# Kernel optimization log

Hardware: AMD Instinct MI355X
Metric: run time of the kernel (lower is better)

Reference implementation:

```python
import jax, jax.numpy as jnp
import numpy as np
import math

B, V, D = 16, 4096, 512
K, H = 64, 8
DK = D // H
DE = 16
DFF = 4 * D
EPS_MASK = 1e-6
EPS_DEN = 1e-8


def setup_inputs() -> dict:
    key = jax.random.key(0)
    ks = jax.random.split(key, 16)
    s = 0.02
    return {
        "x": jax.random.normal(ks[0], (B, V, D), jnp.float32),
        "assign": jax.random.uniform(ks[1], (B, V, K), jnp.float32),
        "E": jax.random.normal(ks[2], (K, DE), jnp.float32),
        "cls0": jax.random.normal(ks[3], (1, K, D), jnp.float32) * s,
        "E2D_w": jax.random.normal(ks[4], (DE, D), jnp.float32) * s,
        "E2D_b": jnp.zeros((D,), jnp.float32),
        "Wq_w": jax.random.normal(ks[5], (D, D), jnp.float32) * s,
        "Wq_b": jnp.zeros((D,), jnp.float32),
        "Wk_w": jax.random.normal(ks[6], (D, D), jnp.float32) * s,
        "Wk_b": jnp.zeros((D,), jnp.float32),
        "Wv_w": jax.random.normal(ks[7], (D, D), jnp.float32) * s,
        "Wv_b": jnp.zeros((D,), jnp.float32),
        "ln_g": jnp.ones((D,), jnp.float32),
        "ln_b": jnp.zeros((D,), jnp.float32),
        "fc1_w": jax.random.normal(ks[8], (D, DFF), jnp.float32) * s,
        "fc1_b": jnp.zeros((DFF,), jnp.float32),
        "fc2_w": jax.random.normal(ks[9], (DFF, D), jnp.float32) * s,
        "fc2_b": jnp.zeros((D,), jnp.float32),
    }


def _layernorm(x, g, b):
    mu = x.mean(-1, keepdims=True)
    var = ((x - mu) ** 2).mean(-1, keepdims=True)
    return (x - mu) / jnp.sqrt(var + 1e-5) * g + b


def reference(x, assign, E, cls0, E2D_w, E2D_b, Wq_w, Wq_b, Wk_w, Wk_b, Wv_w, Wv_b,
              ln_g, ln_b, fc1_w, fc1_b, fc2_w, fc2_b):
    # CLS tokens modulated by module embeddings: [B,K,D]
    cls = jnp.broadcast_to(cls0, (B, K, D)) + (E @ E2D_w + E2D_b)[None]

    # detached mask (transpose of assign): [B,K,V]
    mask_kv = jax.lax.stop_gradient(jnp.swapaxes(assign, 1, 2))
    count_per_k = mask_kv.sum(-1)                 # [B,K]
    empty_mask = count_per_k <= 1e-6              # [B,K]

    # projections -> heads
    q = (_layernorm(cls, ln_g, ln_b) @ Wq_w + Wq_b).reshape(B, K, H, DK)
    k = (x @ Wk_w + Wk_b).reshape(B, V, H, DK)
    v = (x @ Wv_w + Wv_b).reshape(B, V, H, DK)

    # logits [B,H,K,V]
    logits = jnp.einsum("bkhd,bvhd->bhkv", q, k) / math.sqrt(DK)
    log_mask = jnp.log(jnp.clip(mask_kv, 0.0, 1.0) + EPS_MASK)[:, None]  # [B,1,K,V]
    scores = logits + log_mask
    scores = scores - scores.max(-1, keepdims=True)
    attn = jnp.exp(scores)
    attn = attn / (attn.sum(-1, keepdims=True) + EPS_DEN)

    # weighted values, merge heads -> [B,K,D]
    m = jnp.einsum("bhkv,bvhd->bkhd", attn, v).reshape(B, K, D)

    # empty-slot fallback
    m = jnp.where(empty_mask[..., None], cls, m)

    # FFN residual (LayerNorm shared with q path); eval mode: dropout off
    h = _layernorm(m, ln_g, ln_b)
    h = jax.nn.gelu(h @ fc1_w + fc1_b, approximate=False) @ fc2_w + fc2_b
    m = m + h
    return m, count_per_k, empty_mask
```

## Files before the change

### kernel.cpp

```cpp
#include <hip/hip_runtime.h>
#include <hip/hip_bf16.h>
#include <cstdint>
#include <cmath>

#define DEV static __device__ __forceinline__

typedef __attribute__((ext_vector_type(8))) short bf16x8;
typedef __attribute__((ext_vector_type(4))) float f32x4;

DEV ushort f2bf(float f) {
    union { float f; uint32_t u; } v; v.f = f;
    uint32_t r = v.u + 0x7FFFu + ((v.u >> 16) & 1u);
    return (ushort)(r >> 16);
}
DEV uint32_t pack2bf(float lo, float hi) {
    return (uint32_t)f2bf(lo) | ((uint32_t)f2bf(hi) << 16);
}
DEV float bf2f(ushort h) {
    union { uint32_t u; float f; } v; v.u = ((uint32_t)h) << 16;
    return v.f;
}
DEV void gld16(const ushort* g, ushort* l) {
    __builtin_amdgcn_global_load_lds(
        (const __attribute__((address_space(1))) unsigned int*)g,
        (__attribute__((address_space(3))) unsigned int*)l, 16, 0, 0);
}

__global__ __launch_bounds__(256)
void prep_all_k(int nxb, const float* __restrict__ x, ushort* __restrict__ xb,
                const float* __restrict__ E, const float* __restrict__ cls0,
                const float* __restrict__ e2dw, const float* __restrict__ e2db,
                const float* __restrict__ lng, const float* __restrict__ lnbv,
                float* __restrict__ cls, ushort* __restrict__ clsln,
                const float* __restrict__ wk, const float* __restrict__ wv,
                const float* __restrict__ fc1w, const float* __restrict__ fc2w,
                const float* __restrict__ kb, const float* __restrict__ vb,
                ushort* __restrict__ wkvt, ushort* __restrict__ fc1t,
                ushort* __restrict__ fc2t, float* __restrict__ biaskv,
                const float* __restrict__ assign, float* __restrict__ cpart)
{
    __shared__ float sh[64 * 65];
    int id = blockIdx.x;
    const int tid = threadIdx.x;

    if (id < nxb) {
        const size_t i = (size_t)id * 256 + tid;
        const float4* s = (const float4*)(x + i * 8);
        float4 a = s[0], b = s[1];
        uint4 o;
        o.x = pack2bf(a.x, a.y); o.y = pack2bf(a.z, a.w);
        o.z = pack2bf(b.x, b.y); o.w = pack2bf(b.z, b.w);
        *(uint4*)(xb + i * 8) = o;
        return;
    }
    id -= nxb;
    if (id < 64) {
        const int k = id;
        float* Ek = sh + 512;
        float2* red = (float2*)sh;
        if (tid < 16) Ek[tid] = E[k * 16 + tid];
        __syncthreads();
        float vals[2];
#pragma unroll
        for (int j = 0; j < 2; j++) {
            int d = tid + j * 256;
            float a = cls0[k * 512 + d] + e2db[d];
#pragma unroll
            for (int e = 0; e < 16; e++) a += Ek[e] * e2dw[e * 512 + d];
            vals[j] = a;
            cls[k * 512 + d] = a;
        }
        red[tid] = make_float2(vals[0] + vals[1],
                               vals[0] * vals[0] + vals[1] * vals[1]);
        __syncthreads();
        for (int s2 = 128; s2 > 0; s2 >>= 1) {
            if (tid < s2) {
                float2 o = red[tid + s2];
                float2 m = red[tid];
                red[tid] = make_float2(m.x + o.x, m.y + o.y);
            }
            __syncthreads();
        }
        float2 sr = red[0];
        float mu = sr.x * (1.f / 512.f);
        float var = sr.y * (1.f / 512.f) - mu * mu;
        float inv = rsqrtf(var + 1e-5f);
#pragma unroll
        for (int j = 0; j < 2; j++) {
            int d = tid + j * 256;
            clsln[k * 512 + d] = f2bf((vals[j] - mu) * inv * lng[d] + lnbv[d]);
        }
        return;
    }
    id -= 64;
    if (id < 2564) {
        if (id >= 2560) {
            int i = (id - 2560) * 256 + tid;
            biaskv[i] = (i < 512) ? kb[i] : vb[i - 512];
            return;
        }
        const float* in; ushort* out; int R, C, bx, by;
        if (id < 256)        { in = wk;   out = wkvt;             R = 512;  C = 512;  int t = id;        bx = t & 15; by = t >> 4; }
        else if (id < 512)   { in = wv;   out = wkvt + 512 * 512; R = 512;  C = 512;  int t = id - 256;  bx = t & 15; by = t >> 4; }
        else if (id < 1536)  { in = fc1w; out = fc1t;             R = 512;  C = 2048; int t = id - 512;  bx = t & 63; by = t >> 6; }
        else                 { in = fc2w; out = fc2t;             R = 2048; C = 512;  int t = id - 1536; bx = t & 15; by = t >> 4; }
        float (*T)[33] = (float (*)[33])sh;
        const int c0 = bx * 32, r0 = by * 32;
        const int tx = tid & 31, ty = tid >> 5;
#pragma unroll
        for (int i = 0; i < 32; i += 8)
            T[ty + i][tx] = in[(size_t)(r0 + ty + i) * C + c0 + tx];
        __syncthreads();
#pragma unroll
        for (int i = 0; i < 32; i += 8)
            out[(size_t)(c0 + ty + i) * R + r0 + tx] = f2bf(T[tx][ty + i]);
        return;
    }
    id -= 2564;
    {
        const int vt = id & 63, b = id >> 6;
        float (*T)[65] = (float (*)[65])sh;
        const int rr = tid >> 2, sg = tid & 3;
        const float4* src = (const float4*)(assign + ((size_t)b * 4096 + vt * 64 + rr) * 64 + sg * 16);
        float4 a0 = src[0], a1 = src[1], a2 = src[2], a3 = src[3];
        float* tr = &T[rr][sg * 16];
        tr[0] = a0.x; tr[1] = a0.y; tr[2] = a0.z; tr[3] = a0.w;
        tr[4] = a1.x; tr[5] = a1.y; tr[6] = a1.z; tr[7] = a1.w;
        tr[8] = a2.x; tr[9] = a2.y; tr[10] = a2.z; tr[11] = a2.w;
        tr[12] = a3.x; tr[13] = a3.y; tr[14] = a3.z; tr[15] = a3.w;
        __syncthreads();
        const int k = rr;
        float ssum = 0.f;
#pragma unroll
        for (int j = 0; j < 4; j++)
#pragma unroll
            for (int t2 = 0; t2 < 4; t2++) ssum += T[sg * 16 + j * 4 + t2][k];
        ssum += __shfl_xor(ssum, 1, 64);
        ssum += __shfl_xor(ssum, 2, 64);
        if (sg == 0) cpart[((size_t)b * 64 + k) * 64 + vt] = ssum;
    }
}

__global__ __launch_bounds__(512)
void prep_q_k(const ushort* __restrict__ clsln, const float* __restrict__ wq,
              const float* __restrict__ wqb, ushort* __restrict__ qbf)
{
    const int kb = blockIdx.x * 4;
    const int n = threadIdx.x;
    __shared__ float Ar[4][512];
#pragma unroll
    for (int j = 0; j < 4; j++) Ar[j][n] = bf2f(clsln[(kb + j) * 512 + n]);
    __syncthreads();
    float acc[4] = {0.f, 0.f, 0.f, 0.f};
    for (int d = 0; d < 512; ++d) {
        float wv = wq[d * 512 + n];
#pragma unroll
        for (int j = 0; j < 4; j++) acc[j] += Ar[j][d] * wv;
    }
#pragma unroll
    for (int j = 0; j < 4; j++) qbf[(kb + j) * 512 + n] = f2bf(acc[j] + wqb[n]);
}

template<int AMODE, int EPI, int SWZ, int ND, int KD, int LDK>
__global__ __launch_bounds__(512)
void gemm_k(const void* __restrict__ Ap, const ushort* __restrict__ Bt,
            const float* __restrict__ bias,
            ushort* __restrict__ o_bf, const float* __restrict__ res,
            float* __restrict__ o_f)
{
    __shared__ ushort smem[16384];
    ushort* As = smem;
    ushort* Bs = smem + 8192;
    int m0, n0;
    if (SWZ) {
        int L = blockIdx.x;
        int c = L & 7, j = L >> 3;
        m0 = (c * 64 + (j >> 3)) * 128;
        n0 = (j & 7) * 128;
    } else {
        m0 = blockIdx.x * 128;
        n0 = blockIdx.y * 128;
    }
    const int tid = threadIdx.x;
    const int w = tid >> 6, l = tid & 63;
    const int wr = w >> 2, wc = w & 3;
    const int lg = l >> 4, lr = l & 15;

    const f32x4 fzero = {0.f, 0.f, 0.f, 0.f};
    f32x4 acc[4][2];
#pragma unroll
    for (int i = 0; i < 4; i++)
#pragma unroll
        for (int j = 0; j < 2; j++) acc[i][j] = fzero;

    const int lrow8 = l >> 3;
    const int colswz = ((l & 7) ^ lrow8) * 8;
    const ushort* gB  = Bt + (size_t)(n0 + w * 16 + lrow8) * LDK + colswz;
    const ushort* gA0 = (const ushort*)Ap + (size_t)(m0 + w * 16 + lrow8) * LDK + colswz;
    const float*  gA1 = (const float*)Ap + (size_t)(m0 + w * 16 + (l >> 2)) * LDK + (l & 3) * 16;

    const int kbase = blockIdx.z * KD;
    constexpr int NT = KD / 64;
#pragma unroll
    for (int t = 0; t < NT; ++t) {
        const int kt = kbase + t * 64;
        __syncthreads();
        if (AMODE == 0) {
#pragma unroll
            for (int i = 0; i < 2; i++) {
                gld16(gA0 + (size_t)i * 8 * LDK + kt, As + (w * 16 + i * 8) * 64);
                gld16(gB + (size_t)i * 8 * LDK + kt, Bs + (w * 16 + i * 8) * 64);
            }
        } else {
            float4 av[4];
#pragma unroll
            for (int i = 0; i < 4; i++)
                av[i] = *(const float4*)(gA1 + kt + i * 4);
#pragma unroll
            for (int i = 0; i < 2; i++)
                gld16(gB + (size_t)i * 8 * LDK + kt, Bs + (w * 16 + i * 8) * 64);
            {
                int r = w * 16 + (l >> 2);
                uint2 p0, p1;
                p0.x = pack2bf(av[0].x, av[0].y); p0.y = pack2bf(av[0].z, av[0].w);
                uint2 q0; q0.x = pack2bf(av[1].x, av[1].y); q0.y = pack2bf(av[1].z, av[1].w);
                p1.x = pack2bf(av[2].x, av[2].y); p1.y = pack2bf(av[2].z, av[2].w);
                uint2 q1; q1.x = pack2bf(av[3].x, av[3].y); q1.y = pack2bf(av[3].z, av[3].w);
                int cb = (l & 3) * 32;
                *(uint2*)((char*)As + r * 128 + ((cb     ) ^ ((r & 7) << 4))) = p0;
                *(uint2*)((char*)As + r * 128 + ((cb +  8) ^ ((r & 7) << 4))) = q0;
                *(uint2*)((char*)As + r * 128 + ((cb + 16) ^ ((r & 7) << 4))) = p1;
                *(uint2*)((char*)As + r * 128 + ((cb + 24) ^ ((r & 7) << 4))) = q1;
            }
        }
        asm volatile("s_waitcnt vmcnt(0)" ::: "memory");
        __syncthreads();
#pragma unroll
        for (int kk = 0; kk < 2; kk++) {
            int kb = (kk * 32 + lg * 8) * 2;
            bf16x8 af[4], bfv[2];
#pragma unroll
            for (int mi = 0; mi < 4; mi++) {
                int row = wr * 64 + mi * 16 + lr;
                af[mi] = *(bf16x8*)((char*)As + row * 128 + (kb ^ ((row & 7) << 4)));
            }
#pragma unroll
            for (int ni = 0; ni < 2; ni++) {
                int row = wc * 32 + ni * 16 + lr;
                bfv[ni] = *(bf16x8*)((char*)Bs + row * 128 + (kb ^ ((row & 7) << 4)));
            }
#pragma unroll
            for (int mi = 0; mi < 4; mi++)
#pragma unroll
                for (int ni = 0; ni < 2; ni++)
                    acc[mi][ni] = __builtin_amdgcn_mfma_f32_16x16x32_bf16(af[mi], bfv[ni], acc[mi][ni], 0, 0, 0);
        }
    }

    if (EPI == 0) {
        __syncthreads();
#pragma unroll
        for (int mi = 0; mi < 4; mi++)
#pragma unroll
            for (int ni = 0; ni < 2; ni++)
#pragma unroll
                for (int r = 0; r < 4; r++) {
                    int rl = wr * 64 + mi * 16 + lg * 4 + r;
                    int cl = wc * 32 + ni * 16 + lr;
                    int byteoff = rl * 256 + ((cl * 2) ^ ((rl & 7) << 4));
                    *(ushort*)((char*)smem + byteoff) = f2bf(acc[mi][ni][r] + bias[n0 + cl]);
                }
        __syncthreads();
        const int row = tid >> 2, sg2 = tid & 3;
        uint4* dq = (uint4*)(o_bf + (size_t)(m0 + row) * ND + n0 + sg2 * 32);
#pragma unroll
        for (int q2 = 0; q2 < 4; q2++) {
            int byteoff = row * 256 + ((sg2 * 64 + q2 * 16) ^ ((row & 7) << 4));
            dq[q2] = *(const uint4*)((char*)smem + byteoff);
        }
    } else {
        float* ofz = o_f;
        if (EPI == 3)
            ofz = o_f + (size_t)blockIdx.z * (size_t)gridDim.x * 128 * ND;
#pragma unroll
        for (int mi = 0; mi < 4; mi++) {
#pragma unroll
            for (int ni = 0; ni < 2; ni++) {
#pragma unroll
                for (int r = 0; r < 4; r++) {
                    int row = m0 + wr * 64 + mi * 16 + lg * 4 + r;
                    int col = n0 + wc * 32 + ni * 16 + lr;
                    if (EPI == 1) {
                        float c = acc[mi][ni][r] + bias[col];
                        float gg = 0.5f * c * (1.f + erff(c * 0.70710678f));
                        o_bf[(size_t)row * ND + col] = f2bf(gg);
                    } else if (EPI == 2) {
                        float c = acc[mi][ni][r] + bias[col];
                        o_f[(size_t)row * ND + col] = c + res[(size_t)row * ND + col];
                    } else {
                        ofz[(size_t)row * ND + col] = acc[mi][ni][r];
                    }
                }
            }
        }
    }
}

__global__ __launch_bounds__(256)
void combine2_k(const float* __restrict__ fcp, const float* __restrict__ fc2b,
                float* __restrict__ mout)
{
    const int i = blockIdx.x * 256 + threadIdx.x;
    const int col = i & 511;
    float s = fc2b[col] + fcp[i] + fcp[i + 524288] + fcp[i + 2 * 524288] + fcp[i + 3 * 524288];
    mout[i] += s;
}

__global__ __launch_bounds__(256)
void attn_k(const ushort* __restrict__ qbf, const ushort* __restrict__ kv,
            const float* __restrict__ assign,
            float* __restrict__ partO, float* __restrict__ partML)
{
    const int h = blockIdx.x, s = blockIdx.y, b = blockIdx.z;
    __shared__ ushort Qs[64 * 64];
    __shared__ ushort Ks[64 * 64];
    __shared__ ushort Vt[64 * 64];
    __shared__ ushort Ps[64 * 64];
    __shared__ float  Lm[64 * 64];
    const int tid = threadIdx.x;
    const int w = tid >> 6, l = tid & 63, lg = l >> 4, lr = l & 15;
    const int rr = tid >> 2, qt = tid & 3;

    {
        const uint4* src = (const uint4*)(qbf + rr * 512 + h * 64 + qt * 16);
        uint4 t0 = src[0], t1 = src[1];
        int kb = qt * 32;
        *(uint4*)((char*)Qs + rr * 128 + ( kb       ^ ((rr & 7) << 4))) = t0;
        *(uint4*)((char*)Qs + rr * 128 + ((kb + 16) ^ ((rr & 7) << 4))) = t1;
    }

    const f32x4 fzero = {0.f, 0.f, 0.f, 0.f};
    f32x4 oacc[4];
#pragma unroll
    for (int ni = 0; ni < 4; ni++) oacc[ni] = fzero;
    float m_run[4], l_run[4];
#pragma unroll
    for (int r = 0; r < 4; r++) { m_run[r] = -3e38f; l_run[r] = 0.f; }

    const int v00 = s * 512;

    for (int c = 0; c < 8; ++c) {
        const int vb = v00 + c * 64;
        __syncthreads();
        {
            const size_t rowb = ((size_t)b * 4096 + vb + rr) * 1024 + h * 64;
            const uint4* srck = (const uint4*)(kv + rowb + qt * 16);
            uint4 k0 = srck[0], k1 = srck[1];
            int kb = qt * 32;
            *(uint4*)((char*)Ks + rr * 128 + ( kb       ^ ((rr & 7) << 4))) = k0;
            *(uint4*)((char*)Ks + rr * 128 + ((kb + 16) ^ ((rr & 7) << 4))) = k1;
            const ushort* srcv = kv + rowb + 512 + qt * 16;
            ushort vvv[16];
            *(uint4*)&vvv[0] = ((const uint4*)srcv)[0];
            *(uint4*)&vvv[8] = ((const uint4*)srcv)[1];
#pragma unroll
            for (int i = 0; i < 16; i++) {
                int dk = qt * 16 + i;
                *(ushort*)((char*)Vt + dk * 128 + ((rr * 2) ^ ((dk & 7) << 4))) = vvv[i];
            }
            const float4* srca = (const float4*)(assign + ((size_t)b * 4096 + vb + rr) * 64 + qt * 16);
            float4 A0 = srca[0], A1 = srca[1], A2 = srca[2], A3 = srca[3];
            float av[16] = {A0.x, A0.y, A0.z, A0.w, A1.x, A1.y, A1.z, A1.w,
                            A2.x, A2.y, A2.z, A2.w, A3.x, A3.y, A3.z, A3.w};
#pragma unroll
            for (int i = 0; i < 16; i++)
                Lm[(qt * 16 + i) * 64 + rr] = __logf(fminf(fmaxf(av[i], 0.f), 1.f) + 1e-6f);
        }
        __syncthreads();

        f32x4 sacc[4];
#pragma unroll
        for (int ni = 0; ni < 4; ni++) sacc[ni] = fzero;
        __builtin_amdgcn_s_setprio(1);
#pragma unroll
        for (int kk = 0; kk < 2; kk++) {
            int kb = (kk * 32 + lg * 8) * 2;
            int qrow = w * 16 + lr;
            bf16x8 aq = *(bf16x8*)((char*)Qs + qrow * 128 + (kb ^ ((qrow & 7) << 4)));
#pragma unroll
            for (int ni = 0; ni < 4; ni++) {
                int kr = ni * 16 + lr;
                bf16x8 bk = *(bf16x8*)((char*)Ks + kr * 128 + (kb ^ ((kr & 7) << 4)));
                sacc[ni] = __builtin_amdgcn_mfma_f32_16x16x32_bf16(aq, bk, sacc[ni], 0, 0, 0);
            }
        }
        __builtin_amdgcn_s_setprio(0);
        float sv[4][4], mx[4];
#pragma unroll
        for (int r = 0; r < 4; r++) {
            int q = w * 16 + lg * 4 + r;
            float m_ = -3e38f;
#pragma unroll
            for (int ni = 0; ni < 4; ni++) {
                float xx = sacc[ni][r] * 0.125f + Lm[q * 64 + ni * 16 + lr];
                sv[ni][r] = xx;
                m_ = fmaxf(m_, xx);
            }
            mx[r] = m_;
        }
#pragma unroll
        for (int off = 1; off < 16; off <<= 1)
#pragma unroll
            for (int r = 0; r < 4; r++) mx[r] = fmaxf(mx[r], __shfl_xor(mx[r], off, 64));
        float scale[4], lad[4];
#pragma unroll
        for (int r = 0; r < 4; r++) {
            float mn = fmaxf(m_run[r], mx[r]);
            scale[r] = __expf(m_run[r] - mn);
            m_run[r] = mn;
            float ls = 0.f;
#pragma unroll
            for (int ni = 0; ni < 4; ni++) {
                float p = __expf(sv[ni][r] - mn);
                sv[ni][r] = p;
                ls += p;
            }
            lad[r] = ls;
        }
#pragma unroll
        for (int off = 1; off < 16; off <<= 1)
#pragma unroll
            for (int r = 0; r < 4; r++) lad[r] += __shfl_xor(lad[r], off, 64);
#pragma unroll
        for (int r = 0; r < 4; r++) l_run[r] = l_run[r] * scale[r] + lad[r];
#pragma unroll
        for (int ni = 0; ni < 4; ni++) {
            f32x4 o = oacc[ni];
            o[0] *= scale[0]; o[1] *= scale[1]; o[2] *= scale[2]; o[3] *= scale[3];
            oacc[ni] = o;
        }
#pragma unroll
        for (int ni = 0; ni < 4; ni++)
#pragma unroll
            for (int r = 0; r < 4; r++) {
                int q = w * 16 + lg * 4 + r;
                int key = ni * 16 + lr;
                *(ushort*)((char*)Ps + q * 128 + ((key * 2) ^ ((q & 7) << 4))) = f2bf(sv[ni][r]);
            }
        __builtin_amdgcn_s_setprio(1);
#pragma unroll
        for (int kk = 0; kk < 2; kk++) {
            int kb = (kk * 32 + lg * 8) * 2;
            int prow = w * 16 + lr;
            bf16x8 ap = *(bf16x8*)((char*)Ps + prow * 128 + (kb ^ ((prow & 7) << 4)));
#pragma unroll
            for (int ni = 0; ni < 4; ni++) {
                int dk = ni * 16 + lr;
                bf16x8 bv = *(bf16x8*)((char*)Vt + dk * 128 + (kb ^ ((dk & 7) << 4)));
                oacc[ni] = __builtin_amdgcn_mfma_f32_16x16x32_bf16(ap, bv, oacc[ni], 0, 0, 0);
            }
        }
        __builtin_amdgcn_s_setprio(0);
    }
    const size_t ob = ((size_t)((b * 8 + h) * 8 + s)) * 4096;
#pragma unroll
    for (int ni = 0; ni < 4; ni++)
#pragma unroll
        for (int r = 0; r < 4; r++) {
            int q = w * 16 + lg * 4 + r;
            int dk = ni * 16 + lr;
            partO[ob + q * 64 + dk] = oacc[ni][r];
        }
    if (lr == 0) {
#pragma unroll
        for (int r = 0; r < 4; r++) {
            int q = w * 16 + lg * 4 + r;
            partML[((b * 8 + h) * 8 + s) * 128 + q * 2 + 0] = m_run[r];
            partML[((b * 8 + h) * 8 + s) * 128 + q * 2 + 1] = l_run[r];
        }
    }
}

__global__ __launch_bounds__(256)
void combine_k(const float* __restrict__ partO, const float* __restrict__ partML,
               const float* __restrict__ cls, const float* __restrict__ cpart,
               float* __restrict__ cnt, float* __restrict__ emp,
               float* __restrict__ mout)
{
    const int bh = blockIdx.x, b = bh >> 3, h = bh & 7;
    __shared__ float Ms[64], Ls[64], Cs[64];
    const int tid = threadIdx.x;
    if (tid < 64) {
        float M = -3e38f;
#pragma unroll
        for (int s2 = 0; s2 < 8; s2++) M = fmaxf(M, partML[(bh * 8 + s2) * 128 + tid * 2]);
        float L = 0.f;
#pragma unroll
        for (int s2 = 0; s2 < 8; s2++) {
            float m_ = partML[(bh * 8 + s2) * 128 + tid * 2];
            float l_ = partML[(bh * 8 + s2) * 128 + tid * 2 + 1];
            L += l_ * __expf(m_ - M);
        }
        Ms[tid] = M; Ls[tid] = L;
        const float4* p = (const float4*)(cpart + ((size_t)b * 64 + tid) * 64);
        float cs = 0.f;
#pragma unroll
        for (int t = 0; t < 16; t++) {
            float4 f = p[t];
            cs += f.x + f.y + f.z + f.w;
        }
        Cs[tid] = cs;
        if (h == 0) {
            cnt[b * 64 + tid] = cs;
            emp[b * 64 + tid] = (cs <= 1e-6f) ? 1.f : 0.f;
        }
    }
    __syncthreads();
#pragma unroll
    for (int i = 0; i < 16; i++) {
        int e = i * 256 + tid;
        int q = e >> 6, dk = e & 63;
        float o = 0.f;
#pragma unroll
        for (int s2 = 0; s2 < 8; s2++) {
            float m_ = partML[(bh * 8 + s2) * 128 + q * 2];
            o += partO[(size_t)(bh * 8 + s2) * 4096 + e] * __expf(m_ - Ms[q]);
        }
        float val = o / (Ls[q] + 1e-8f);
        if (Cs[q] <= 1e-6f) val = cls[q * 512 + h * 64 + dk];
        mout[((size_t)b * 64 + q) * 512 + h * 64 + dk] = val;
    }
}

__global__ __launch_bounds__(256)
void ln_rows_k(const float* __restrict__ m, const float* __restrict__ g,
               const float* __restrict__ be, ushort* __restrict__ out)
{
    const int r = blockIdx.x, tid = threadIdx.x;
    float v0 = m[(size_t)r * 512 + tid];
    float v1 = m[(size_t)r * 512 + tid + 256];
    __shared__ float2 red[256];
    red[tid] = make_float2(v0 + v1, v0 * v0 + v1 * v1);
    __syncthreads();
    for (int s2 = 128; s2 > 0; s2 >>= 1) {
        if (tid < s2) {
            float2 o = red[tid + s2];
            float2 m2 = red[tid];
            red[tid] = make_float2(m2.x + o.x, m2.y + o.y);
        }
        __syncthreads();
    }
    float2 sr = red[0];
    float mu = sr.x * (1.f / 512.f);
    float var = sr.y * (1.f / 512.f) - mu * mu;
    float inv = rsqrtf(var + 1e-5f);
    out[(size_t)r * 512 + tid]       = f2bf((v0 - mu) * inv * g[tid] + be[tid]);
    out[(size_t)r * 512 + tid + 256] = f2bf((v1 - mu) * inv * g[tid + 256] + be[tid + 256]);
}

extern "C" void kernel_launch(void* const* d_in, const int* in_sizes, int n_in,
                              void* d_out, int out_size, void* d_ws, size_t ws_size,
                              hipStream_t stream)
{
    const float* x      = (const float*)d_in[0];
    const float* assign = (const float*)d_in[1];
    const float* E      = (const float*)d_in[2];
    const float* cls0   = (const float*)d_in[3];
    const float* e2dw   = (const float*)d_in[4];
    const float* e2db   = (const float*)d_in[5];
    const float* wq     = (const float*)d_in[6];
    const float* wqb    = (const float*)d_in[7];
    const float* wk     = (const float*)d_in[8];
    const float* wkb    = (const float*)d_in[9];
    const float* wv     = (const float*)d_in[10];
    const float* wvb    = (const float*)d_in[11];
    const float* lng    = (const float*)d_in[12];
    const float* lnbv   = (const float*)d_in[13];
    const float* fc1w   = (const float*)d_in[14];
    const float* fc1b   = (const float*)d_in[15];
    const float* fc2w   = (const float*)d_in[16];
    const float* fc2b   = (const float*)d_in[17];

    float* mout = (float*)d_out;
    float* cnt  = mout + (size_t)16 * 64 * 512;
    float* emp  = cnt + 16 * 64;

    char* ws = (char*)d_ws;
    size_t off = 0;
    auto alloc = [&](size_t bytes) -> char* {
        char* p = ws + off;
        off = (off + bytes + 255) & ~(size_t)255;
        return p;
    };
    float*  cls    = (float*) alloc((size_t)64 * 512 * 4);
    ushort* clsln  = (ushort*)alloc((size_t)64 * 512 * 2);
    ushort* qbf    = (ushort*)alloc((size_t)64 * 512 * 2);
    ushort* wkvt   = (ushort*)alloc((size_t)1024 * 512 * 2);
    float*  biaskv = (float*) alloc((size_t)1024 * 4);
    ushort* fc1t   = (ushort*)alloc((size_t)2048 * 512 * 2);
    ushort* fc2t   = (ushort*)alloc((size_t)512 * 2048 * 2);
    ushort* kvb    = (ushort*)alloc((size_t)16 * 4096 * 1024 * 2);
    float*  partO  = (float*) alloc((size_t)16 * 8 * 8 * 64 * 64 * 4);
    float*  partML = (float*) alloc((size_t)16 * 8 * 8 * 64 * 2 * 4);
    float*  cpart  = (float*) alloc((size_t)16 * 64 * 64 * 4);
    ushort* lnbf   = (ushort*)alloc((size_t)1024 * 512 * 2);
    ushort* hhb    = (ushort*)alloc((size_t)1024 * 2048 * 2);
    float*  fcp    = (float*) alloc((size_t)4 * 1024 * 512 * 4);
    ushort* xb     = (ushort*)alloc((size_t)16 * 4096 * 512 * 2);
    const bool use_xb = (off <= ws_size);

    const int nxb = use_xb ? 16384 : 0;
    prep_all_k<<<nxb + 64 + 2564 + 1024, 256, 0, stream>>>(
        nxb, x, xb, E, cls0, e2dw, e2db, lng, lnbv, cls, clsln,
        wk, wv, fc1w, fc2w, wkb, wvb, wkvt, fc1t, fc2t, biaskv,
        assign, cpart);
    prep_q_k<<<16, 512, 0, stream>>>(clsln, wq, wqb, qbf);

    if (use_xb) {
        gemm_k<0, 0, 1, 1024, 512, 512><<<4096, 512, 0, stream>>>(xb, wkvt, biaskv,
                                                                  kvb, nullptr, nullptr);
    } else {
        gemm_k<1, 0, 1, 1024, 512, 512><<<4096, 512, 0, stream>>>(x, wkvt, biaskv,
                                                                  kvb, nullptr, nullptr);
    }
    attn_k<<<dim3(8, 8, 16), 256, 0, stream>>>(qbf, kvb, assign, partO, partML);
    combine_k<<<128, 256, 0, stream>>>(partO, partML, cls, cpart, cnt, emp, mout);
    ln_rows_k<<<1024, 256, 0, stream>>>(mout, lng, lnbv, lnbf);
    gemm_k<0, 1, 0, 2048, 512, 512><<<dim3(8, 16), 512, 0, stream>>>(lnbf, fc1t, fc1b,
                                                                     hhb, nullptr, nullptr);
    gemm_k<0, 3, 0, 512, 512, 2048><<<dim3(8, 4, 4), 512, 0, stream>>>(hhb, fc2t, fc2b,
                                                                       nullptr, nullptr, fcp);
    combine2_k<<<2048, 256, 0, stream>>>(fcp, fc2b, mout);
}
```

Measured before the change: 279.6 us.

## Fuse Q projection into prep kernel and halve attention split-V count

Each CLS-row block in the prep kernel now keeps its layernormed row in fp32 shared memory and computes the Q projection itself, so the separate prep_q_k launch and the bf16 clsln buffer go away. The attention kernel now splits V into 4 chunks of 1024 instead of 8 of 512, which halves the partial outputs that the combine step must merge. The trade-off is that 64 prep blocks each run a serial 512x512 dot-product loop, which may lengthen the prep tail, and the attention grid shrinks to 512 blocks, which lowers occupancy. Q is also no longer rounded to bf16 after layernorm, a small numerical change.

```diff
diff --git a/kernel.cpp b/kernel.cpp
--- a/kernel.cpp
+++ b/kernel.cpp
@@ -31,7 +31,8 @@
                 const float* __restrict__ E, const float* __restrict__ cls0,
                 const float* __restrict__ e2dw, const float* __restrict__ e2db,
                 const float* __restrict__ lng, const float* __restrict__ lnbv,
-                float* __restrict__ cls, ushort* __restrict__ clsln,
+                const float* __restrict__ wq, const float* __restrict__ wqb,
+                float* __restrict__ cls, ushort* __restrict__ qbf,
                 const float* __restrict__ wk, const float* __restrict__ wv,
                 const float* __restrict__ fc1w, const float* __restrict__ fc2w,
                 const float* __restrict__ kb, const float* __restrict__ vb,
@@ -56,8 +57,9 @@
     id -= nxb;
     if (id < 64) {
         const int k = id;
+        float* lnv = sh;
         float* Ek = sh + 512;
-        float2* red = (float2*)sh;
+        float2* red = (float2*)(sh + 544);
         if (tid < 16) Ek[tid] = E[k * 16 + tid];
         __syncthreads();
         float vals[2];
@@ -85,10 +87,20 @@
         float mu = sr.x * (1.f / 512.f);
         float var = sr.y * (1.f / 512.f) - mu * mu;
         float inv = rsqrtf(var + 1e-5f);
+        __syncthreads();
 #pragma unroll
         for (int j = 0; j < 2; j++) {
             int d = tid + j * 256;
-            clsln[k * 512 + d] = f2bf((vals[j] - mu) * inv * lng[d] + lnbv[d]);
+            lnv[d] = (vals[j] - mu) * inv * lng[d] + lnbv[d];
+        }
+        __syncthreads();
+#pragma unroll
+        for (int j = 0; j < 2; j++) {
+            int n = tid + j * 256;
+            float acc = 0.f;
+            for (int d = 0; d < 512; ++d)
+                acc += lnv[d] * wq[d * 512 + n];
+            qbf[k * 512 + n] = f2bf(acc + wqb[n]);
         }
         return;
     }
@@ -139,26 +151,6 @@
         ssum += __shfl_xor(ssum, 2, 64);
         if (sg == 0) cpart[((size_t)b * 64 + k) * 64 + vt] = ssum;
     }
-}
-
-__global__ __launch_bounds__(512)
-void prep_q_k(const ushort* __restrict__ clsln, const float* __restrict__ wq,
-              const float* __restrict__ wqb, ushort* __restrict__ qbf)
-{
-    const int kb = blockIdx.x * 4;
-    const int n = threadIdx.x;
-    __shared__ float Ar[4][512];
-#pragma unroll
-    for (int j = 0; j < 4; j++) Ar[j][n] = bf2f(clsln[(kb + j) * 512 + n]);
-    __syncthreads();
-    float acc[4] = {0.f, 0.f, 0.f, 0.f};
-    for (int d = 0; d < 512; ++d) {
-        float wv = wq[d * 512 + n];
-#pragma unroll
-        for (int j = 0; j < 4; j++) acc[j] += Ar[j][d] * wv;
-    }
-#pragma unroll
-    for (int j = 0; j < 4; j++) qbf[(kb + j) * 512 + n] = f2bf(acc[j] + wqb[n]);
 }
 
 template<int AMODE, int EPI, int SWZ, int ND, int KD, int LDK>
@@ -347,9 +339,9 @@
 #pragma unroll
     for (int r = 0; r < 4; r++) { m_run[r] = -3e38f; l_run[r] = 0.f; }
 
-    const int v00 = s * 512;
-
-    for (int c = 0; c < 8; ++c) {
+    const int v00 = s * 1024;
+
+    for (int c = 0; c < 16; ++c) {
         const int vb = v00 + c * 64;
         __syncthreads();
         {
@@ -462,7 +454,7 @@
         }
         __builtin_amdgcn_s_setprio(0);
     }
-    const size_t ob = ((size_t)((b * 8 + h) * 8 + s)) * 4096;
+    const size_t ob = ((size_t)((b * 8 + h) * 4 + s)) * 4096;
 #pragma unroll
     for (int ni = 0; ni < 4; ni++)
 #pragma unroll
@@ -475,8 +467,8 @@
 #pragma unroll
         for (int r = 0; r < 4; r++) {
             int q = w * 16 + lg * 4 + r;
-            partML[((b * 8 + h) * 8 + s) * 128 + q * 2 + 0] = m_run[r];
-            partML[((b * 8 + h) * 8 + s) * 128 + q * 2 + 1] = l_run[r];
+            partML[((b * 8 + h) * 4 + s) * 128 + q * 2 + 0] = m_run[r];
+            partML[((b * 8 + h) * 4 + s) * 128 + q * 2 + 1] = l_run[r];
         }
     }
 }
@@ -493,12 +485,12 @@
     if (tid < 64) {
         float M = -3e38f;
 #pragma unroll
-        for (int s2 = 0; s2 < 8; s2++) M = fmaxf(M, partML[(bh * 8 + s2) * 128 + tid * 2]);
+        for (int s2 = 0; s2 < 4; s2++) M = fmaxf(M, partML[(bh * 4 + s2) * 128 + tid * 2]);
         float L = 0.f;
 #pragma unroll
-        for (int s2 = 0; s2 < 8; s2++) {
-            float m_ = partML[(bh * 8 + s2) * 128 + tid * 2];
-            float l_ = partML[(bh * 8 + s2) * 128 + tid * 2 + 1];
+        for (int s2 = 0; s2 < 4; s2++) {
+            float m_ = partML[(bh * 4 + s2) * 128 + tid * 2];
+            float l_ = partML[(bh * 4 + s2) * 128 + tid * 2 + 1];
             L += l_ * __expf(m_ - M);
         }
         Ms[tid] = M; Ls[tid] = L;
@@ -522,9 +514,9 @@
         int q = e >> 6, dk = e & 63;
         float o = 0.f;
 #pragma unroll
-        for (int s2 = 0; s2 < 8; s2++) {
-            float m_ = partML[(bh * 8 + s2) * 128 + q * 2];
-            o += partO[(size_t)(bh * 8 + s2) * 4096 + e] * __expf(m_ - Ms[q]);
+        for (int s2 = 0; s2 < 4; s2++) {
+            float m_ = partML[(bh * 4 + s2) * 128 + q * 2];
+            o += partO[(size_t)(bh * 4 + s2) * 4096 + e] * __expf(m_ - Ms[q]);
         }
         float val = o / (Ls[q] + 1e-8f);
         if (Cs[q] <= 1e-6f) val = cls[q * 512 + h * 64 + dk];
@@ -593,15 +585,14 @@
         return p;
     };
     float*  cls    = (float*) alloc((size_t)64 * 512 * 4);
-    ushort* clsln  = (ushort*)alloc((size_t)64 * 512 * 2);
     ushort* qbf    = (ushort*)alloc((size_t)64 * 512 * 2);
     ushort* wkvt   = (ushort*)alloc((size_t)1024 * 512 * 2);
     float*  biaskv = (float*) alloc((size_t)1024 * 4);
     ushort* fc1t   = (ushort*)alloc((size_t)2048 * 512 * 2);
     ushort* fc2t   = (ushort*)alloc((size_t)512 * 2048 * 2);
     ushort* kvb    = (ushort*)alloc((size_t)16 * 4096 * 1024 * 2);
-    float*  partO  = (float*) alloc((size_t)16 * 8 * 8 * 64 * 64 * 4);
-    float*  partML = (float*) alloc((size_t)16 * 8 * 8 * 64 * 2 * 4);
+    float*  partO  = (float*) alloc((size_t)16 * 8 * 4 * 64 * 64 * 4);
+    float*  partML = (float*) alloc((size_t)16 * 8 * 4 * 128 * 4);
     float*  cpart  = (float*) alloc((size_t)16 * 64 * 64 * 4);
     ushort* lnbf   = (ushort*)alloc((size_t)1024 * 512 * 2);
     ushort* hhb    = (ushort*)alloc((size_t)1024 * 2048 * 2);
@@ -611,10 +602,9 @@
 
     const int nxb = use_xb ? 16384 : 0;
     prep_all_k<<<nxb + 64 + 2564 + 1024, 256, 0, stream>>>(
-        nxb, x, xb, E, cls0, e2dw, e2db, lng, lnbv, cls, clsln,
+        nxb, x, xb, E, cls0, e2dw, e2db, lng, lnbv, wq, wqb, cls, qbf,
         wk, wv, fc1w, fc2w, wkb, wvb, wkvt, fc1t, fc2t, biaskv,
         assign, cpart);
-    prep_q_k<<<16, 512, 0, stream>>>(clsln, wq, wqb, qbf);
 
     if (use_xb) {
         gemm_k<0, 0, 1, 1024, 512, 512><<<4096, 512, 0, stream>>>(xb, wkvt, biaskv,
@@ -623,7 +613,7 @@
         gemm_k<1, 0, 1, 1024, 512, 512><<<4096, 512, 0, stream>>>(x, wkvt, biaskv,
                                                                   kvb, nullptr, nullptr);
     }
-    attn_k<<<dim3(8, 8, 16), 256, 0, stream>>>(qbf, kvb, assign, partO, partML);
+    attn_k<<<dim3(8, 4, 16), 256, 0, stream>>>(qbf, kvb, assign, partO, partML);
     combine_k<<<128, 256, 0, stream>>>(partO, partML, cls, cpart, cnt, emp, mout);
     ln_rows_k<<<1024, 256, 0, stream>>>(mout, lng, lnbv, lnbf);
     gemm_k<0, 1, 0, 2048, 512, 512><<<dim3(8, 16), 512, 0, stream>>>(lnbf, fc1t, fc1b,
```

New measurement: 275.0 us, median of 2. No clear change (-1.6%).
